# Kernel tuning notes

Measured on AMD Instinct MI355X. Metric: run time of the kernel, lower is better.

The kernel has to match this reference:

```python
import jax, jax.numpy as jnp
import numpy as np

PAD_TOKEN_ID = 0
EPS = 1e-12  # torch F.normalize eps

B_Q, L_Q = 64, 32
B_D, L_D = 512, 256
HID, OUT = 768, 128
VOCAB = 30522


def setup_inputs() -> dict:
    key = jax.random.key(0)
    k1, k2, k3, k4, k5 = jax.random.split(key, 5)
    return {
        "q_hidden": jax.random.normal(k1, (B_Q, L_Q, HID), dtype=jnp.float32),
        "d_hidden": jax.random.normal(k2, (B_D, L_D, HID), dtype=jnp.float32),
        "d_input_ids": jax.random.randint(k3, (B_D, L_D), 0, VOCAB, dtype=jnp.int32),
        "skiplist": jax.random.randint(k4, (64,), 0, VOCAB, dtype=jnp.int32),
        "W": jax.random.normal(k5, (OUT, HID), dtype=jnp.float32) * (HID ** -0.5),
    }


def _l2norm(x):
    n = jnp.sqrt(jnp.sum(x * x, axis=-1, keepdims=True))
    return x / jnp.maximum(n, EPS)


def reference(q_hidden, d_hidden, d_input_ids, skiplist, W):
    # query(): linear proj + L2 normalize      (B_q, L_q, F)
    Q = _l2norm(jnp.einsum("blh,fh->blf", q_hidden, W))
    # doc(): linear proj + L2 normalize + mask (B_d, L_d, F)
    D = _l2norm(jnp.einsum("blh,fh->blf", d_hidden, W))
    is_pad = d_input_ids == PAD_TOKEN_ID
    is_punct = jnp.any(d_input_ids[..., None] == skiplist, axis=-1)
    d_mask = (~is_pad) & (~is_punct)                     # (B_d, L_d)
    D = D * d_mask[..., None].astype(D.dtype)
    # forward(): reshape to (B, N, L, F) with B = min(B_q, B_d)
    B = min(q_hidden.shape[0], d_hidden.shape[0])
    Qr = Q.reshape(B, -1, L_Q, OUT)                      # (B, 1, L_q, F)
    Dr = D.reshape(B, -1, L_D, OUT)                      # (B, N_p, L_d, F)
    Mr = d_mask.reshape(B, -1, L_D)                      # (B, N_p, L_d)
    # similarity(): cosine MaxSim, Q @ D^T with broadcast over N_p
    sim = jnp.einsum("bqf,bndf->bnqd", Qr[:, 0], Dr)     # (B, N_p, L_q, L_d)
    sim = jnp.where(Mr[:, :, None, :], sim, -jnp.inf)
    sms = jnp.max(sim, axis=-1).mean(axis=-1)            # (B, N_p)
    return sms
```

## Files before the change

kernel.cpp:

```cpp
#include <hip/hip_runtime.h>
#include <stdint.h>

typedef float  f32x4 __attribute__((ext_vector_type(4)));
typedef short  s16x8 __attribute__((ext_vector_type(8)));
typedef unsigned int u32;
typedef unsigned short u16;
typedef unsigned int u32x4 __attribute__((ext_vector_type(4)));

#define HID 768
#define OUTF 128
#define LQ 32
#define LD 256

__device__ __forceinline__ u32 pk_rna(float lo, float hi) {
    u32 a = __builtin_bit_cast(u32, lo) + 0x8000u;
    u32 b = __builtin_bit_cast(u32, hi) + 0x8000u;
    return __builtin_amdgcn_perm(b, a, 0x07060302u);
}
__device__ __forceinline__ u16 f2bf(float x) {
    return (u16)((__builtin_bit_cast(u32, x) + 0x8000u) >> 16);
}
__device__ __forceinline__ s16x8 cvt8(f32x4 lo, f32x4 hi) {
    union { u32 u[4]; s16x8 v; } ua;
    ua.u[0] = pk_rna(lo[0], lo[1]);
    ua.u[1] = pk_rna(lo[2], lo[3]);
    ua.u[2] = pk_rna(hi[0], hi[1]);
    ua.u[3] = pk_rna(hi[2], hi[3]);
    return ua.v;
}

__global__ __launch_bounds__(256) void wconv(const float* __restrict__ W,
                                             u32* __restrict__ Wb3d) {
    int t = blockIdx.x * 256 + threadIdx.x;
    int j2   = t & 3;
    int lane = (t >> 2) & 63;
    int cf   = (t >> 8) & 7;
    int kk   = t >> 11;
    int l15 = lane & 15, g4 = lane >> 4;
    int f = cf * 16 + l15;
    int k = kk * 32 + g4 * 8 + j2 * 2;
    const float* src = W + (size_t)f * HID + k;
    Wb3d[t] = pk_rna(src[0], src[1]);
}

__global__ __launch_bounds__(256) void qproj(const float* __restrict__ qh,
                                             const u16* __restrict__ Wb3,
                                             u16* __restrict__ Qb) {
    const int b = blockIdx.x;
    const int tid = threadIdx.x;
    const int w = tid >> 6, lane = tid & 63, g = lane >> 4, l15 = lane & 15;

    f32x4 acc[2][2] = {};
    const float* A0 = qh + ((size_t)b * LQ + l15) * HID + g * 8;
    const float* A1 = A0 + 16 * HID;
    const u16* Bp = Wb3 + w * 1024 + lane * 8;

    for (int kk = 0; kk < 24; ++kk) {
        f32x4 x0 = *(const f32x4*)A0;
        f32x4 x1 = *(const f32x4*)(A0 + 4);
        f32x4 y0 = *(const f32x4*)A1;
        f32x4 y1 = *(const f32x4*)(A1 + 4);
        s16x8 b0 = *(const s16x8*)(Bp);
        s16x8 b1 = *(const s16x8*)(Bp + 512);
        s16x8 a0 = cvt8(x0, x1);
        s16x8 a1 = cvt8(y0, y1);
        acc[0][0] = __builtin_amdgcn_mfma_f32_16x16x32_bf16(a0, b0, acc[0][0], 0, 0, 0);
        acc[0][1] = __builtin_amdgcn_mfma_f32_16x16x32_bf16(a0, b1, acc[0][1], 0, 0, 0);
        acc[1][0] = __builtin_amdgcn_mfma_f32_16x16x32_bf16(a1, b0, acc[1][0], 0, 0, 0);
        acc[1][1] = __builtin_amdgcn_mfma_f32_16x16x32_bf16(a1, b1, acc[1][1], 0, 0, 0);
        A0 += 32; A1 += 32; Bp += 4096;
    }

    __shared__ float part[4][32];
    __shared__ float invl[32];
#pragma unroll
    for (int rf = 0; rf < 2; ++rf)
#pragma unroll
        for (int reg = 0; reg < 4; ++reg) {
            float ss = acc[rf][0][reg] * acc[rf][0][reg] + acc[rf][1][reg] * acc[rf][1][reg];
            ss += __shfl_xor(ss, 1); ss += __shfl_xor(ss, 2);
            ss += __shfl_xor(ss, 4); ss += __shfl_xor(ss, 8);
            if (l15 == 0) part[w][rf * 16 + g * 4 + reg] = ss;
        }
    __syncthreads();
    if (tid < 32) {
        float ss = part[0][tid] + part[1][tid] + part[2][tid] + part[3][tid];
        invl[tid] = 1.f / fmaxf(sqrtf(ss), 1e-12f);
    }
    __syncthreads();
#pragma unroll
    for (int rf = 0; rf < 2; ++rf)
#pragma unroll
        for (int cf = 0; cf < 2; ++cf)
#pragma unroll
            for (int reg = 0; reg < 4; ++reg) {
                int q = rf * 16 + g * 4 + reg;
                int f = w * 32 + cf * 16 + l15;
                Qb[(size_t)b * LQ * OUTF + q * OUTF + f] = f2bf(acc[rf][cf][reg] * invl[q]);
            }
}

__global__ __launch_bounds__(512, 2) void dmax(const float* __restrict__ dh,
                                               const int* __restrict__ ids,
                                               const int* __restrict__ skiplist,
                                               const u16* __restrict__ Wb3,
                                               const u16* __restrict__ Qb,
                                               float* __restrict__ out) {
    const int bid = blockIdx.x;
    const int tid = threadIdx.x;
    const int w = tid >> 6, lane = tid & 63, g4 = lane >> 4, l15 = lane & 15;
    const int qh_ = w >> 2;

    __shared__ __align__(16) u16 stg[3][12288];
    __shared__ __align__(16) u16 outb[2][2048];
    __shared__ __align__(16) float nrm[2][16][8];
    __shared__ float wsum[8];
    __shared__ int ms[512];
    __shared__ int sk[64];

#define PADOF(v) (((v) / 192) * 1536 + (((((v) % 192)) * 8) ^ ((((v) / 192) & 7) << 4)))
    const int pad0 = PADOF(2 * tid), pad1 = PADOF(2 * tid + 1024), pad2 = PADOF(2 * tid + 2048);

    const int swz = (l15 & 7) << 4, sw45 = swz & 48, sw6 = swz & 64;
    const int aoffE = l15 * 1536 + ((g4 * 16) ^ sw45) + sw6;
    const int aoffO = l15 * 1536 + ((g4 * 16) ^ sw45) + 64 - sw6;
    const int doffE = l15 * 256 + ((g4 * 16) ^ sw45) + sw6;
    const int doffO = l15 * 256 + ((g4 * 16) ^ sw45) + 64 - sw6;

    f32x4 LA0, LA1, LA2, LA3, LA4, LA5, LB0, LB1, LB2, LB3, LB4, LB5,
          LC0, LC1, LC2, LC3, LC4, LC5;
    s16x8 Qr0, Qr1, Qr2, Qr3;
    float rmaxH[4] = {-INFINITY, -INFINITY, -INFINITY, -INFINITY};

#define SLABBASE(sab) ((const char*)dh + (size_t)(bid + (((sab) >> 4) << 8)) * 786432 \
                       + (size_t)((sab) & 15) * 49152)

#define LISSUE(sab, S) { const char* gb_ = SLABBASE(sab) + 32 * tid; \
    S##0 = *(const f32x4*)(gb_);          S##1 = *(const f32x4*)(gb_ + 16); \
    S##2 = *(const f32x4*)(gb_ + 16384);  S##3 = *(const f32x4*)(gb_ + 16400); \
    S##4 = *(const f32x4*)(gb_ + 32768);  S##5 = *(const f32x4*)(gb_ + 32784); }

#define WSTORE(P, S) { char* sb_ = (char*)&stg[P][0]; u32x4 q_; \
    q_[0] = pk_rna(S##0[0], S##0[1]); q_[1] = pk_rna(S##0[2], S##0[3]); \
    q_[2] = pk_rna(S##1[0], S##1[1]); q_[3] = pk_rna(S##1[2], S##1[3]); \
    *(u32x4*)(sb_ + pad0) = q_; \
    q_[0] = pk_rna(S##2[0], S##2[1]); q_[1] = pk_rna(S##2[2], S##2[3]); \
    q_[2] = pk_rna(S##3[0], S##3[1]); q_[3] = pk_rna(S##3[2], S##3[3]); \
    *(u32x4*)(sb_ + pad1) = q_; \
    q_[0] = pk_rna(S##4[0], S##4[1]); q_[1] = pk_rna(S##4[2], S##4[3]); \
    q_[2] = pk_rna(S##5[0], S##5[1]); q_[3] = pk_rna(S##5[2], S##5[3]); \
    *(u32x4*)(sb_ + pad2) = q_; }

#define QLOAD(doc_) { const u16* qp_ = Qb + (size_t)((bid + (doc_) * 256) >> 3) * 4096 \
                      + (qh_ * 16 + l15) * 128 + g4 * 8; \
    Qr0 = *(const s16x8*)(qp_);      Qr1 = *(const s16x8*)(qp_ + 32); \
    Qr2 = *(const s16x8*)(qp_ + 64); Qr3 = *(const s16x8*)(qp_ + 96); }

#define GEMMN(P, s_) { \
    const char* Ab_ = (const char*)&stg[P][0]; \
    u16* ob_ = &outb[(s_) & 1][0]; \
    f32x4 ac0_ = {}, ac1_ = {}; \
    _Pragma("unroll") for (int kkp = 0; kkp < 12; ++kkp) { \
        s16x8 ae_ = *(const s16x8*)(Ab_ + aoffE + kkp * 128); \
        s16x8 ao_ = *(const s16x8*)(Ab_ + aoffO + kkp * 128); \
        ac0_ = __builtin_amdgcn_mfma_f32_16x16x32_bf16(ae_, Bf[2 * kkp],     ac0_, 0, 0, 0); \
        ac1_ = __builtin_amdgcn_mfma_f32_16x16x32_bf16(ao_, Bf[2 * kkp + 1], ac1_, 0, 0, 0); \
    } \
    f32x4 aG_ = ac0_ + ac1_; \
    _Pragma("unroll") for (int rg = 0; rg < 4; ++rg) { \
        float ss_ = aG_[rg] * aG_[rg]; \
        ss_ += __shfl_xor(ss_, 1); ss_ += __shfl_xor(ss_, 2); \
        ss_ += __shfl_xor(ss_, 4); ss_ += __shfl_xor(ss_, 8); \
        if (l15 == 0) nrm[(s_) & 1][g4 * 4 + rg][w] = ss_; \
        int dr_ = g4 * 4 + rg; \
        int of_ = (dr_ * 256 + (w * 16 + l15) * 2) ^ ((dr_ & 7) << 4); \
        *(u16*)((char*)ob_ + of_) = f2bf(aG_[rg]); \
    } }

#define TAIL(sb) { \
    if ((w & 3) == 0) { \
        const char* Db_ = (const char*)&outb[(sb) & 1][0]; \
        s16x8 d0_ = *(const s16x8*)(Db_ + doffE); \
        s16x8 d1_ = *(const s16x8*)(Db_ + doffO); \
        s16x8 d2_ = *(const s16x8*)(Db_ + doffE + 128); \
        s16x8 d3_ = *(const s16x8*)(Db_ + doffO + 128); \
        f32x4 s2_ = {}; \
        s2_ = __builtin_amdgcn_mfma_f32_16x16x32_bf16(Qr0, d0_, s2_, 0, 0, 0); \
        s2_ = __builtin_amdgcn_mfma_f32_16x16x32_bf16(Qr1, d1_, s2_, 0, 0, 0); \
        s2_ = __builtin_amdgcn_mfma_f32_16x16x32_bf16(Qr2, d2_, s2_, 0, 0, 0); \
        s2_ = __builtin_amdgcn_mfma_f32_16x16x32_bf16(Qr3, d3_, s2_, 0, 0, 0); \
        f32x4 n0_ = *(const f32x4*)&nrm[(sb) & 1][l15][0]; \
        f32x4 n1_ = *(const f32x4*)&nrm[(sb) & 1][l15][4]; \
        float ssv_ = (n0_[0] + n0_[1] + n0_[2] + n0_[3]) \
                   + (n1_[0] + n1_[1] + n1_[2] + n1_[3]); \
        float inv_ = 1.f / fmaxf(sqrtf(ssv_), 1e-12f); \
        int keep_ = ms[(((sb) >> 4) << 8) + (((sb) & 15) << 4) + l15]; \
        _Pragma("unroll") for (int rg = 0; rg < 4; ++rg) { \
            float v_ = keep_ ? s2_[rg] * inv_ : -INFINITY; \
            rmaxH[rg] = fmaxf(rmaxH[rg], v_); } \
    } \
    if (((sb) & 15) == 15) { \
        if ((w & 3) == 0) { \
            float ps_ = 0.f; \
            _Pragma("unroll") for (int rg = 0; rg < 4; ++rg) { \
                float v_ = rmaxH[rg]; \
                v_ = fmaxf(v_, __shfl_xor(v_, 1)); v_ = fmaxf(v_, __shfl_xor(v_, 2)); \
                v_ = fmaxf(v_, __shfl_xor(v_, 4)); v_ = fmaxf(v_, __shfl_xor(v_, 8)); \
                ps_ += v_; rmaxH[rg] = -INFINITY; } \
            ps_ += __shfl_xor(ps_, 16); ps_ += __shfl_xor(ps_, 32); \
            if (lane == 0) wsum[w] = ps_; \
            if ((sb) == 15) { QLOAD(1); } \
        } \
        asm volatile("s_waitcnt lgkmcnt(0)" ::: "memory"); \
        __builtin_amdgcn_s_barrier(); \
        if (tid == 0) out[bid + (((sb) >> 4) << 8)] = (wsum[0] + wsum[4]) * (1.f / 32.f); \
    } }

#define SLABSTEP(s_, PG_, PW_, RN_, RW_, doIssue_, doWr_) { \
    if (doIssue_) LISSUE((s_) + 3, RN_); \
    if (doWr_) WSTORE(PW_, RW_); \
    GEMMN(PG_, s_); \
    asm volatile("s_waitcnt lgkmcnt(0)" ::: "memory"); \
    __builtin_amdgcn_s_barrier(); \
    TAIL(s_); }

    LISSUE(0, LA);
    LISSUE(1, LB);
    LISSUE(2, LC);

    s16x8 Bf[24];
#pragma unroll
    for (int kk = 0; kk < 24; ++kk)
        Bf[kk] = *(const s16x8*)(Wb3 + (size_t)(kk * 8 + w) * 512 + lane * 8);

    if (tid < 64) sk[tid] = skiplist[tid];
    asm volatile("s_waitcnt lgkmcnt(0)" ::: "memory");
    __builtin_amdgcn_s_barrier();
    {
        int d_ = tid >> 8, r_ = tid & 255;
        int id_ = ids[(size_t)(bid + d_ * 256) * 256 + r_];
        int keep_ = (id_ != 0);
#pragma unroll
        for (int j = 0; j < 64; ++j) keep_ &= (id_ != sk[j]);
        ms[tid] = keep_;
    }
    WSTORE(0, LA);
    if ((w & 3) == 0) { QLOAD(0); }
    asm volatile("s_waitcnt lgkmcnt(0)" ::: "memory");
    __builtin_amdgcn_s_barrier();

    for (int j = 0; j < 10; ++j) {
        const int s0 = 3 * j;
        SLABSTEP(s0,     0, 1, LA, LB, true,        true);
        SLABSTEP(s0 + 1, 1, 2, LB, LC, true,        true);
        SLABSTEP(s0 + 2, 2, 0, LC, LA, s0 + 5 < 32, true);
    }
    SLABSTEP(30, 0, 1, LA, LB, false, true);
    SLABSTEP(31, 1, 2, LB, LC, false, false);
}

extern "C" void kernel_launch(void* const* d_in, const int* in_sizes, int n_in,
                              void* d_out, int out_size, void* d_ws, size_t ws_size,
                              hipStream_t stream) {
    const float* q_hidden = (const float*)d_in[0];
    const float* d_hidden = (const float*)d_in[1];
    const int*   d_ids    = (const int*)d_in[2];
    const int*   skiplist = (const int*)d_in[3];
    const float* W        = (const float*)d_in[4];
    float* out = (float*)d_out;

    u16* Wb3 = (u16*)d_ws;
    u16* Qb  = (u16*)((char*)d_ws + 256 * 1024);

    wconv<<<192, 256, 0, stream>>>(W, (u32*)Wb3);
    qproj<<<64, 256, 0, stream>>>(q_hidden, Wb3, Qb);
    dmax<<<256, 512, 0, stream>>>(d_hidden, d_ids, skiplist, Wb3, Qb, out);
}
```

Before: 103.2 us.

## Deepen slab pipeline to four stages and spread MaxSim tails across warps

Restructures the dmax loop from a three-stage, one-slab-per-barrier pipeline into a four-buffer scheme that handles two slabs per barrier, which halves the number of block barriers. The Q·D MaxSim tail work is now round-robined over warp groups instead of always landing on warps 0 and 4, and a shared-memory FLUSH combines the per-warp maxima at each document boundary. The aim is to cut barrier stalls and the serialisation of tail work behind the projection GEMM. In exchange, LDS use grows and four sets of prefetch registers are held live, which raises register pressure and risks spills or lower occupancy.

Measured after the change: 148.2 us. 43.6% more time.

```diff
diff --git a/kernel.cpp b/kernel.cpp
--- a/kernel.cpp
+++ b/kernel.cpp
@@ -111,10 +111,10 @@
     const int w = tid >> 6, lane = tid & 63, g4 = lane >> 4, l15 = lane & 15;
     const int qh_ = w >> 2;
 
-    __shared__ __align__(16) u16 stg[3][12288];
-    __shared__ __align__(16) u16 outb[2][2048];
-    __shared__ __align__(16) float nrm[2][16][8];
-    __shared__ float wsum[8];
+    __shared__ __align__(16) u16 stg[4][12288];
+    __shared__ __align__(16) u16 outb[4][2048];
+    __shared__ __align__(16) float nrm[4][16][8];
+    __shared__ float red[8][16];
     __shared__ int ms[512];
     __shared__ int sk[64];
 
@@ -127,8 +127,10 @@
     const int doffE = l15 * 256 + ((g4 * 16) ^ sw45) + sw6;
     const int doffO = l15 * 256 + ((g4 * 16) ^ sw45) + 64 - sw6;
 
-    f32x4 LA0, LA1, LA2, LA3, LA4, LA5, LB0, LB1, LB2, LB3, LB4, LB5,
-          LC0, LC1, LC2, LC3, LC4, LC5;
+    f32x4 P0_0, P0_1, P0_2, P0_3, P0_4, P0_5,
+          P1_0, P1_1, P1_2, P1_3, P1_4, P1_5,
+          P2_0, P2_1, P2_2, P2_3, P2_4, P2_5,
+          P3_0, P3_1, P3_2, P3_3, P3_4, P3_5;
     s16x8 Qr0, Qr1, Qr2, Qr3;
     float rmaxH[4] = {-INFINITY, -INFINITY, -INFINITY, -INFINITY};
 
@@ -136,19 +138,19 @@
                        + (size_t)((sab) & 15) * 49152)
 
 #define LISSUE(sab, S) { const char* gb_ = SLABBASE(sab) + 32 * tid; \
-    S##0 = *(const f32x4*)(gb_);          S##1 = *(const f32x4*)(gb_ + 16); \
-    S##2 = *(const f32x4*)(gb_ + 16384);  S##3 = *(const f32x4*)(gb_ + 16400); \
-    S##4 = *(const f32x4*)(gb_ + 32768);  S##5 = *(const f32x4*)(gb_ + 32784); }
+    S##_0 = *(const f32x4*)(gb_);          S##_1 = *(const f32x4*)(gb_ + 16); \
+    S##_2 = *(const f32x4*)(gb_ + 16384);  S##_3 = *(const f32x4*)(gb_ + 16400); \
+    S##_4 = *(const f32x4*)(gb_ + 32768);  S##_5 = *(const f32x4*)(gb_ + 32784); }
 
 #define WSTORE(P, S) { char* sb_ = (char*)&stg[P][0]; u32x4 q_; \
-    q_[0] = pk_rna(S##0[0], S##0[1]); q_[1] = pk_rna(S##0[2], S##0[3]); \
-    q_[2] = pk_rna(S##1[0], S##1[1]); q_[3] = pk_rna(S##1[2], S##1[3]); \
+    q_[0] = pk_rna(S##_0[0], S##_0[1]); q_[1] = pk_rna(S##_0[2], S##_0[3]); \
+    q_[2] = pk_rna(S##_1[0], S##_1[1]); q_[3] = pk_rna(S##_1[2], S##_1[3]); \
     *(u32x4*)(sb_ + pad0) = q_; \
-    q_[0] = pk_rna(S##2[0], S##2[1]); q_[1] = pk_rna(S##2[2], S##2[3]); \
-    q_[2] = pk_rna(S##3[0], S##3[1]); q_[3] = pk_rna(S##3[2], S##3[3]); \
+    q_[0] = pk_rna(S##_2[0], S##_2[1]); q_[1] = pk_rna(S##_2[2], S##_2[3]); \
+    q_[2] = pk_rna(S##_3[0], S##_3[1]); q_[3] = pk_rna(S##_3[2], S##_3[3]); \
     *(u32x4*)(sb_ + pad1) = q_; \
-    q_[0] = pk_rna(S##4[0], S##4[1]); q_[1] = pk_rna(S##4[2], S##4[3]); \
-    q_[2] = pk_rna(S##5[0], S##5[1]); q_[3] = pk_rna(S##5[2], S##5[3]); \
+    q_[0] = pk_rna(S##_4[0], S##_4[1]); q_[1] = pk_rna(S##_4[2], S##_4[3]); \
+    q_[2] = pk_rna(S##_5[0], S##_5[1]); q_[3] = pk_rna(S##_5[2], S##_5[3]); \
     *(u32x4*)(sb_ + pad2) = q_; }
 
 #define QLOAD(doc_) { const u16* qp_ = Qb + (size_t)((bid + (doc_) * 256) >> 3) * 4096 \
@@ -156,9 +158,9 @@
     Qr0 = *(const s16x8*)(qp_);      Qr1 = *(const s16x8*)(qp_ + 32); \
     Qr2 = *(const s16x8*)(qp_ + 64); Qr3 = *(const s16x8*)(qp_ + 96); }
 
-#define GEMMN(P, s_) { \
-    const char* Ab_ = (const char*)&stg[P][0]; \
-    u16* ob_ = &outb[(s_) & 1][0]; \
+#define GEMMN(PS, OB) { \
+    const char* Ab_ = (const char*)&stg[PS][0]; \
+    u16* ob_ = &outb[OB][0]; \
     f32x4 ac0_ = {}, ac1_ = {}; \
     _Pragma("unroll") for (int kkp = 0; kkp < 12; ++kkp) { \
         s16x8 ae_ = *(const s16x8*)(Ab_ + aoffE + kkp * 128); \
@@ -171,15 +173,15 @@
         float ss_ = aG_[rg] * aG_[rg]; \
         ss_ += __shfl_xor(ss_, 1); ss_ += __shfl_xor(ss_, 2); \
         ss_ += __shfl_xor(ss_, 4); ss_ += __shfl_xor(ss_, 8); \
-        if (l15 == 0) nrm[(s_) & 1][g4 * 4 + rg][w] = ss_; \
+        if (l15 == 0) nrm[OB][g4 * 4 + rg][w] = ss_; \
         int dr_ = g4 * 4 + rg; \
         int of_ = (dr_ * 256 + (w * 16 + l15) * 2) ^ ((dr_ & 7) << 4); \
         *(u16*)((char*)ob_ + of_) = f2bf(aG_[rg]); \
     } }
 
-#define TAIL(sb) { \
-    if ((w & 3) == 0) { \
-        const char* Db_ = (const char*)&outb[(sb) & 1][0]; \
+#define TAILRR(s_, OB, PR) { \
+    if ((w & 3) == (PR)) { \
+        const char* Db_ = (const char*)&outb[OB][0]; \
         s16x8 d0_ = *(const s16x8*)(Db_ + doffE); \
         s16x8 d1_ = *(const s16x8*)(Db_ + doffO); \
         s16x8 d2_ = *(const s16x8*)(Db_ + doffE + 128); \
@@ -189,44 +191,38 @@
         s2_ = __builtin_amdgcn_mfma_f32_16x16x32_bf16(Qr1, d1_, s2_, 0, 0, 0); \
         s2_ = __builtin_amdgcn_mfma_f32_16x16x32_bf16(Qr2, d2_, s2_, 0, 0, 0); \
         s2_ = __builtin_amdgcn_mfma_f32_16x16x32_bf16(Qr3, d3_, s2_, 0, 0, 0); \
-        f32x4 n0_ = *(const f32x4*)&nrm[(sb) & 1][l15][0]; \
-        f32x4 n1_ = *(const f32x4*)&nrm[(sb) & 1][l15][4]; \
+        f32x4 n0_ = *(const f32x4*)&nrm[OB][l15][0]; \
+        f32x4 n1_ = *(const f32x4*)&nrm[OB][l15][4]; \
         float ssv_ = (n0_[0] + n0_[1] + n0_[2] + n0_[3]) \
                    + (n1_[0] + n1_[1] + n1_[2] + n1_[3]); \
         float inv_ = 1.f / fmaxf(sqrtf(ssv_), 1e-12f); \
-        int keep_ = ms[(((sb) >> 4) << 8) + (((sb) & 15) << 4) + l15]; \
+        int keep_ = ms[(((s_) >> 4) << 8) + (((s_) & 15) << 4) + l15]; \
         _Pragma("unroll") for (int rg = 0; rg < 4; ++rg) { \
             float v_ = keep_ ? s2_[rg] * inv_ : -INFINITY; \
             rmaxH[rg] = fmaxf(rmaxH[rg], v_); } \
-    } \
-    if (((sb) & 15) == 15) { \
-        if ((w & 3) == 0) { \
-            float ps_ = 0.f; \
-            _Pragma("unroll") for (int rg = 0; rg < 4; ++rg) { \
-                float v_ = rmaxH[rg]; \
-                v_ = fmaxf(v_, __shfl_xor(v_, 1)); v_ = fmaxf(v_, __shfl_xor(v_, 2)); \
-                v_ = fmaxf(v_, __shfl_xor(v_, 4)); v_ = fmaxf(v_, __shfl_xor(v_, 8)); \
-                ps_ += v_; rmaxH[rg] = -INFINITY; } \
-            ps_ += __shfl_xor(ps_, 16); ps_ += __shfl_xor(ps_, 32); \
-            if (lane == 0) wsum[w] = ps_; \
-            if ((sb) == 15) { QLOAD(1); } \
-        } \
-        asm volatile("s_waitcnt lgkmcnt(0)" ::: "memory"); \
-        __builtin_amdgcn_s_barrier(); \
-        if (tid == 0) out[bid + (((sb) >> 4) << 8)] = (wsum[0] + wsum[4]) * (1.f / 32.f); \
     } }
 
-#define SLABSTEP(s_, PG_, PW_, RN_, RW_, doIssue_, doWr_) { \
-    if (doIssue_) LISSUE((s_) + 3, RN_); \
-    if (doWr_) WSTORE(PW_, RW_); \
-    GEMMN(PG_, s_); \
+#define FLUSH(doc_) { \
+    _Pragma("unroll") for (int rg = 0; rg < 4; ++rg) { \
+        float v_ = rmaxH[rg]; \
+        v_ = fmaxf(v_, __shfl_xor(v_, 1)); v_ = fmaxf(v_, __shfl_xor(v_, 2)); \
+        v_ = fmaxf(v_, __shfl_xor(v_, 4)); v_ = fmaxf(v_, __shfl_xor(v_, 8)); \
+        if (l15 == 0) red[w][g4 * 4 + rg] = v_; \
+        rmaxH[rg] = -INFINITY; } \
     asm volatile("s_waitcnt lgkmcnt(0)" ::: "memory"); \
     __builtin_amdgcn_s_barrier(); \
-    TAIL(s_); }
-
-    LISSUE(0, LA);
-    LISSUE(1, LB);
-    LISSUE(2, LC);
+    if (tid < 32) { \
+        int l_ = tid & 15; \
+        int base_ = (tid < 16) ? 0 : 4; \
+        float m_ = fmaxf(fmaxf(red[base_][l_], red[base_ + 1][l_]), \
+                         fmaxf(red[base_ + 2][l_], red[base_ + 3][l_])); \
+        m_ += __shfl_xor(m_, 1); m_ += __shfl_xor(m_, 2); \
+        m_ += __shfl_xor(m_, 4); m_ += __shfl_xor(m_, 8); \
+        m_ += __shfl_xor(m_, 16); \
+        if (tid == 0) out[bid + (doc_) * 256] = m_ * (1.f / 32.f); } }
+
+    LISSUE(0, P0);
+    LISSUE(1, P1);
 
     s16x8 Bf[24];
 #pragma unroll
@@ -234,6 +230,11 @@
         Bf[kk] = *(const s16x8*)(Wb3 + (size_t)(kk * 8 + w) * 512 + lane * 8);
 
     if (tid < 64) sk[tid] = skiplist[tid];
+    WSTORE(0, P0);
+    WSTORE(1, P1);
+    LISSUE(2, P2);
+    LISSUE(3, P3);
+    QLOAD(0);
     asm volatile("s_waitcnt lgkmcnt(0)" ::: "memory");
     __builtin_amdgcn_s_barrier();
     {
@@ -244,19 +245,38 @@
         for (int j = 0; j < 64; ++j) keep_ &= (id_ != sk[j]);
         ms[tid] = keep_;
     }
-    WSTORE(0, LA);
-    if ((w & 3) == 0) { QLOAD(0); }
-    asm volatile("s_waitcnt lgkmcnt(0)" ::: "memory");
-    __builtin_amdgcn_s_barrier();
-
-    for (int j = 0; j < 10; ++j) {
-        const int s0 = 3 * j;
-        SLABSTEP(s0,     0, 1, LA, LB, true,        true);
-        SLABSTEP(s0 + 1, 1, 2, LB, LC, true,        true);
-        SLABSTEP(s0 + 2, 2, 0, LC, LA, s0 + 5 < 32, true);
-    }
-    SLABSTEP(30, 0, 1, LA, LB, false, true);
-    SLABSTEP(31, 1, 2, LB, LC, false, false);
+
+    for (int jj = 0; jj < 8; ++jj) {
+        if (jj > 0) {
+            TAILRR(4 * jj - 2, 2, 2);
+            TAILRR(4 * jj - 1, 3, 3);
+        }
+        if (jj == 4) { FLUSH(0); QLOAD(1); }
+        WSTORE(2, P2);
+        WSTORE(3, P3);
+        if (jj < 7) { LISSUE(4 * jj + 4, P0); LISSUE(4 * jj + 5, P1); }
+        GEMMN(0, 0);
+        GEMMN(1, 1);
+        asm volatile("s_waitcnt lgkmcnt(0)" ::: "memory");
+        __builtin_amdgcn_s_barrier();
+
+        TAILRR(4 * jj, 0, 0);
+        TAILRR(4 * jj + 1, 1, 1);
+        if (jj < 7) {
+            WSTORE(0, P0);
+            WSTORE(1, P1);
+            LISSUE(4 * jj + 6, P2);
+            LISSUE(4 * jj + 7, P3);
+        }
+        GEMMN(2, 2);
+        GEMMN(3, 3);
+        asm volatile("s_waitcnt lgkmcnt(0)" ::: "memory");
+        __builtin_amdgcn_s_barrier();
+    }
+
+    TAILRR(30, 2, 2);
+    TAILRR(31, 3, 3);
+    FLUSH(1);
 }
 
 extern "C" void kernel_launch(void* const* d_in, const int* in_sizes, int n_in,
```
